# Optimization experiments

Measured on AMD Instinct MI355X. Metric: run time of the kernel, lower is better.

## Reference

```python
import jax, jax.numpy as jnp
import numpy as np

NUM_HEADS = 16
EPS = 1e-5
CHUNK = 128  # chunk length for the chunked recurrent-state scan


def _linear_attention(x, Wq, Wk, Wv, Wo, bo):
    B, T, E = x.shape
    H = NUM_HEADS
    d = E // H

    def proj(W):
        # nn.Linear(bias=False): y = x @ W.T ; split heads -> (B,H,T,d)
        return (x @ W.T).reshape(B, T, H, d).transpose(0, 2, 1, 3)

    phi_q = jax.nn.elu(proj(Wq)) + 1.0
    phi_k = jax.nn.elu(proj(Wk)) + 1.0
    V = proj(Wv)

    nC = T // CHUNK
    # (nC, B, H, C, d) so lax.scan iterates over chunks of time
    def to_chunks(a):
        return a.reshape(B, H, nC, CHUNK, d).transpose(2, 0, 1, 3, 4)

    qc, kc, vc = to_chunks(phi_q), to_chunks(phi_k), to_chunks(V)
    mask = jnp.tril(jnp.ones((CHUNK, CHUNK), x.dtype))  # causal incl. diagonal

    S0 = jnp.zeros((B, H, d, d), x.dtype)  # running sum of k v^T
    z0 = jnp.zeros((B, H, d), x.dtype)     # running sum of phi_k

    def step(carry, inp):
        S, z = carry
        q, k, v = inp  # (B,H,C,d)
        A = jnp.einsum('bhid,bhjd->bhij', q, k) * mask
        num = jnp.einsum('bhij,bhjd->bhid', A, v) + jnp.einsum('bhid,bhde->bhie', q, S)
        den = jnp.sum(A, axis=-1) + jnp.einsum('bhid,bhd->bhi', q, z) + EPS
        out = num / den[..., None]
        S = S + jnp.einsum('bhjd,bhje->bhde', k, v)
        z = z + jnp.sum(k, axis=2)
        return (S, z), out

    _, outs = jax.lax.scan(step, (S0, z0), (qc, kc, vc))  # (nC,B,H,C,d)
    out = outs.transpose(1, 2, 0, 3, 4).reshape(B, H, T, d)
    out = out.transpose(0, 2, 1, 3).reshape(B, T, E)
    # out_proj (dropout p=0 / eval -> identity)
    return out @ Wo.T + bo


def setup_inputs() -> dict:
    key = jax.random.key(0)
    ks = jax.random.split(key, 6)
    B, T, E = 2, 2048, 1024
    s = 1.0 / np.sqrt(E)
    return {
        'x': jax.random.normal(ks[0], (B, T, E), jnp.float32),
        'Wq': jax.random.normal(ks[1], (E, E), jnp.float32) * s,
        'Wk': jax.random.normal(ks[2], (E, E), jnp.float32) * s,
        'Wv': jax.random.normal(ks[3], (E, E), jnp.float32) * s,
        'Wo': jax.random.normal(ks[4], (E, E), jnp.float32) * s,
        'bo': jnp.zeros((E,), jnp.float32),
    }


def reference(x, Wq, Wk, Wv, Wo, bo):
    return _linear_attention(x, Wq, Wk, Wv, Wo, bo)
```

## Files before the change

kernel.cpp:

```cpp
#include <hip/hip_runtime.h>
#include <hip/hip_bf16.h>
#include <stdint.h>

typedef __attribute__((ext_vector_type(4)))  float  floatx4;
typedef __attribute__((ext_vector_type(8)))  short  short8;
typedef __attribute__((ext_vector_type(8)))  unsigned short ushortx8;
typedef __attribute__((ext_vector_type(4)))  unsigned short ushortx4;

#define B_  2
#define T_  2048
#define E_  1024
#define H_  16
#define D_  64
#define C_  128
#define NC_ 16
#define M_  4096
#define EPS_ 1e-5f

__device__ __forceinline__ unsigned short f2b(float f) {
    union { float f; unsigned int u; } v; v.f = f;
    unsigned int r = v.u + 0x7fffu + ((v.u >> 16) & 1u);
    return (unsigned short)(r >> 16);
}
__device__ __forceinline__ float b2f(unsigned short b) {
    union { unsigned int u; float f; } v; v.u = ((unsigned int)b) << 16;
    return v.f;
}

__device__ __forceinline__ int stage_seg(int i) { return (i & 3) ^ ((i >> 3) & 3); }
__device__ __forceinline__ int frag_slot(int lane) {
    int m = lane & 15, q = lane >> 4;
    return m * 4 + (q ^ ((m >> 1) & 3));
}

__global__ __launch_bounds__(256) void convert_all(const float* __restrict__ x,
                                                   const float* __restrict__ Wq,
                                                   const float* __restrict__ Wk,
                                                   const float* __restrict__ Wv,
                                                   const float* __restrict__ Wo,
                                                   unsigned short* __restrict__ dst) {
    int i = (blockIdx.x * 256 + threadIdx.x) * 4;
    const float* s; int off;
    if (i < M_ * E_) { s = x; off = i; }
    else {
        int j = i - M_ * E_;
        int which = j >> 20;
        s = (which == 0) ? Wq : (which == 1) ? Wk : (which == 2) ? Wv : Wo;
        off = j & ((1 << 20) - 1);
    }
    float4 f = *(const float4*)(s + off);
    ushortx4 o;
    o[0] = f2b(f.x); o[1] = f2b(f.y); o[2] = f2b(f.z); o[3] = f2b(f.w);
    *(ushortx4*)(dst + i) = o;
}

__global__ __launch_bounds__(256) void gemm_qkv(const unsigned short* __restrict__ A,
                                                const unsigned short* __restrict__ Bm,
                                                unsigned short* __restrict__ Cb) {
    const int N = 3 * E_, K = E_;
    __shared__ __align__(16) unsigned short smem[32768];
    unsigned short* at0 = smem;
    unsigned short* bt0 = smem + 8192;
    unsigned short* at1 = smem + 16384;
    unsigned short* bt1 = smem + 24576;
    int tid = threadIdx.x;
    int wave = tid >> 6, lane = tid & 63;
    int wr = wave >> 1, wc = wave & 1;
    int m = lane & 15, q = lane >> 4;
    int srow = lane >> 2, sseg = stage_seg(lane);
    int fs = frag_slot(lane);
    int row0 = blockIdx.y * 128, col0 = blockIdx.x * 128;
    floatx4 acc[4][4];
    for (int i = 0; i < 4; i++) for (int j = 0; j < 4; j++) acc[i][j] = floatx4{0.f, 0.f, 0.f, 0.f};

    auto stageA = [&](unsigned short* at, int k0) {
        for (int p = 0; p < 4; p++) {
            int t = p * 4 + wave;
            const unsigned short* ga = A + (size_t)(row0 + (t & 7) * 16 + srow) * K + k0 + (t >> 3) * 32 + sseg * 8;
            __builtin_amdgcn_global_load_lds((const __attribute__((address_space(1))) unsigned int*)ga,
                (__attribute__((address_space(3))) unsigned int*)(at + t * 512), 16, 0, 0);
        }
    };
    auto stageB = [&](unsigned short* bt, int k0) {
        for (int p = 0; p < 4; p++) {
            int u = p * 4 + wave;
            const unsigned short* gb = Bm + (size_t)(col0 + (u & 7) * 16 + srow) * K + k0 + (u >> 3) * 32 + sseg * 8;
            __builtin_amdgcn_global_load_lds((const __attribute__((address_space(1))) unsigned int*)gb,
                (__attribute__((address_space(3))) unsigned int*)(bt + u * 512), 16, 0, 0);
        }
    };
    short8 af[4], bf[4];
    auto frags = [&](const unsigned short* at, const unsigned short* bt, int kh) {
        for (int mi = 0; mi < 4; mi++) af[mi] = *(const short8*)(at + (kh * 8 + wr * 4 + mi) * 512 + fs * 8);
        for (int ni = 0; ni < 4; ni++) bf[ni] = *(const short8*)(bt + (kh * 8 + wc * 4 + ni) * 512 + fs * 8);
    };
    auto mfma16 = [&]() {
        __builtin_amdgcn_s_setprio(1);
        for (int mi = 0; mi < 4; mi++)
            for (int ni = 0; ni < 4; ni++)
                acc[mi][ni] = __builtin_amdgcn_mfma_f32_16x16x32_bf16(af[mi], bf[ni], acc[mi][ni], 0, 0, 0);
        __builtin_amdgcn_s_setprio(0);
    };

    stageA(at0, 0); stageB(bt0, 0);
    for (int k0 = 0; k0 < K; k0 += 128) {
        stageA(at1, k0 + 64);
        asm volatile("s_waitcnt vmcnt(4)" ::: "memory");
        __builtin_amdgcn_s_barrier();
        frags(at0, bt0, 0);
        mfma16();
        frags(at0, bt0, 1);
        stageB(bt1, k0 + 64);
        mfma16();
        __builtin_amdgcn_s_barrier();
        if (k0 + 128 < K) {
            stageA(at0, k0 + 128);
            asm volatile("s_waitcnt vmcnt(4)" ::: "memory");
        } else {
            asm volatile("s_waitcnt vmcnt(0)" ::: "memory");
        }
        __builtin_amdgcn_s_barrier();
        frags(at1, bt1, 0);
        mfma16();
        frags(at1, bt1, 1);
        if (k0 + 128 < K) stageB(bt0, k0 + 128);
        mfma16();
        __builtin_amdgcn_s_barrier();
    }

    unsigned short* epi = smem + wave * 2176;
    bool isphi = (col0 < 2 * E_);
    for (int half = 0; half < 2; half++) {
        if (half) asm volatile("" ::: "memory");
        for (int mi2 = 0; mi2 < 2; mi2++) {
            int mi = half * 2 + mi2;
            for (int ni = 0; ni < 4; ni++)
                for (int reg = 0; reg < 4; reg++) {
                    int lr = mi2 * 16 + q * 4 + reg;
                    float v = acc[mi][ni][reg];
                    if (isphi) v = (v > 0.f) ? (v + 1.f) : __expf(v);
                    epi[lr * 68 + ni * 16 + m] = f2b(v);
                }
        }
        for (int i = 0; i < 4; i++) {
            int s = i * 64 + lane;
            int lr = s >> 3, seg = s & 7;
            const unsigned short* p = epi + lr * 68 + seg * 8;
            ushortx4 lo = *(const ushortx4*)(p);
            ushortx4 hi = *(const ushortx4*)(p + 4);
            ushortx8 val;
            for (int e = 0; e < 4; e++) { val[e] = lo[e]; val[e + 4] = hi[e]; }
            int row = row0 + wr * 64 + half * 32 + lr;
            int col = col0 + wc * 64 + seg * 8;
            *(ushortx8*)(Cb + (size_t)row * N + col) = val;
        }
    }
}

__global__ __launch_bounds__(256) void gemm_out(const unsigned short* __restrict__ A,
                                                const unsigned short* __restrict__ Bm,
                                                const float* __restrict__ bias,
                                                float* __restrict__ Cf) {
    const int N = E_, K = E_;
    __shared__ __align__(16) unsigned short smem[24576];
    unsigned short* at0 = smem;
    unsigned short* bt0 = smem + 8192;
    unsigned short* at1 = smem + 12288;
    unsigned short* bt1 = smem + 20480;
    int tid = threadIdx.x;
    int wave = tid >> 6, lane = tid & 63;
    int wr = wave >> 1, wc = wave & 1;
    int m = lane & 15, q = lane >> 4;
    int srow = lane >> 2, sseg = stage_seg(lane);
    int fs = frag_slot(lane);
    int row0 = blockIdx.y * 128, col0 = blockIdx.x * 64;
    floatx4 acc[4][2];
    for (int i = 0; i < 4; i++) for (int j = 0; j < 2; j++) acc[i][j] = floatx4{0.f, 0.f, 0.f, 0.f};

    auto stageA = [&](unsigned short* at, int k0) {
        for (int p = 0; p < 4; p++) {
            int t = p * 4 + wave;
            const unsigned short* ga = A + (size_t)(row0 + (t & 7) * 16 + srow) * K + k0 + (t >> 3) * 32 + sseg * 8;
            __builtin_amdgcn_global_load_lds((const __attribute__((address_space(1))) unsigned int*)ga,
                (__attribute__((address_space(3))) unsigned int*)(at + t * 512), 16, 0, 0);
        }
    };
    auto stageB = [&](unsigned short* bt, int k0) {
        for (int p = 0; p < 2; p++) {
            int u = p * 4 + wave;
            const unsigned short* gb = Bm + (size_t)(col0 + (u & 3) * 16 + srow) * K + k0 + (u >> 2) * 32 + sseg * 8;
            __builtin_amdgcn_global_load_lds((const __attribute__((address_space(1))) unsigned int*)gb,
                (__attribute__((address_space(3))) unsigned int*)(bt + u * 512), 16, 0, 0);
        }
    };
    short8 af[4], bf[2];
    auto frags = [&](const unsigned short* at, const unsigned short* bt, int kh) {
        for (int mi = 0; mi < 4; mi++) af[mi] = *(const short8*)(at + (kh * 8 + wr * 4 + mi) * 512 + fs * 8);
        for (int ci = 0; ci < 2; ci++) bf[ci] = *(const short8*)(bt + (kh * 4 + wc * 2 + ci) * 512 + fs * 8);
    };
    auto mfma8 = [&]() {
        __builtin_amdgcn_s_setprio(1);
        for (int mi = 0; mi < 4; mi++)
            for (int ci = 0; ci < 2; ci++)
                acc[mi][ci] = __builtin_amdgcn_mfma_f32_16x16x32_bf16(af[mi], bf[ci], acc[mi][ci], 0, 0, 0);
        __builtin_amdgcn_s_setprio(0);
    };

    stageA(at0, 0); stageB(bt0, 0);
    for (int k0 = 0; k0 < K; k0 += 128) {
        stageA(at1, k0 + 64);
        asm volatile("s_waitcnt vmcnt(4)" ::: "memory");
        __builtin_amdgcn_s_barrier();
        frags(at0, bt0, 0);
        mfma8();
        frags(at0, bt0, 1);
        stageB(bt1, k0 + 64);
        mfma8();
        __builtin_amdgcn_s_barrier();
        if (k0 + 128 < K) {
            stageA(at0, k0 + 128);
            asm volatile("s_waitcnt vmcnt(4)" ::: "memory");
        } else {
            asm volatile("s_waitcnt vmcnt(0)" ::: "memory");
        }
        __builtin_amdgcn_s_barrier();
        frags(at1, bt1, 0);
        mfma8();
        frags(at1, bt1, 1);
        if (k0 + 128 < K) stageB(bt0, k0 + 128);
        mfma8();
        __builtin_amdgcn_s_barrier();
    }

    int qrow = q * 4;
    for (int ci = 0; ci < 2; ci++) {
        int col = col0 + wc * 32 + ci * 16 + m;
        float bv = bias[col];
        for (int mi = 0; mi < 4; mi++)
            for (int r2 = 0; r2 < 4; r2++) {
                int row = row0 + wr * 64 + mi * 16 + qrow + r2;
                Cf[(size_t)row * N + col] = acc[mi][ci][r2] + bv;
            }
    }
}

__global__ __launch_bounds__(256) void chunk_sums(const unsigned short* __restrict__ qkv,
                                                  float* __restrict__ Sc, float* __restrict__ zc) {
    int c = blockIdx.x, h = blockIdx.y, bb = blockIdx.z;
    __shared__ __align__(16) unsigned short Kt[64 * 132];
    __shared__ __align__(16) unsigned short Vt[80 * 132];
    int tid = threadIdx.x;
    int lane = tid & 63, w = tid >> 6;
    size_t rowb = (size_t)bb * T_ + (size_t)c * C_;
    int kcol = E_ + h * D_, vcol = 2 * E_ + h * D_;

    {
        int r4 = (tid >> 3) * 4;
        int seg = (tid & 7) * 8;
        ushortx8 kv[4], vv[4];
        for (int t = 0; t < 4; t++) {
            size_t g = (rowb + r4 + t) * 3072;
            kv[t] = *(const ushortx8*)(qkv + g + kcol + seg);
            vv[t] = *(const ushortx8*)(qkv + g + vcol + seg);
        }
        for (int e = 0; e < 8; e++) {
            ushortx4 ka, va;
            for (int t = 0; t < 4; t++) { ka[t] = kv[t][e]; va[t] = vv[t][e]; }
            *(ushortx4*)(Kt + (seg + e) * 132 + r4) = ka;
            *(ushortx4*)(Vt + (seg + e) * 132 + r4) = va;
        }
    }
    if (tid < 128) Vt[64 * 132 + tid] = 0x3f80;
    __syncthreads();

    floatx4 acc[5];
    for (int ni = 0; ni < 5; ni++) acc[ni] = floatx4{0.f, 0.f, 0.f, 0.f};
    int lm = lane & 15, lk = (lane >> 4) * 8;
    for (int k0 = 0; k0 < 128; k0 += 32) {
        short8 af = *(const short8*)(Kt + (w * 16 + lm) * 132 + k0 + lk);
        for (int ni = 0; ni < 5; ni++) {
            short8 bf = *(const short8*)(Vt + (ni * 16 + lm) * 132 + k0 + lk);
            acc[ni] = __builtin_amdgcn_mfma_f32_16x16x32_bf16(af, bf, acc[ni], 0, 0, 0);
        }
    }
    size_t base = ((size_t)(bb * H_ + h) * NC_ + c) * (size_t)(D_ * D_);
    int r0 = w * 16 + (lane >> 4) * 4;
    for (int ni = 0; ni < 4; ni++)
        for (int reg = 0; reg < 4; reg++)
            Sc[base + (size_t)(r0 + reg) * D_ + ni * 16 + lm] = acc[ni][reg];
    if (lm == 0) {
        size_t zb = ((size_t)(bb * H_ + h) * NC_ + c) * D_;
        for (int reg = 0; reg < 4; reg++) zc[zb + r0 + reg] = acc[4][reg];
    }
}

__global__ __launch_bounds__(256) void attn_kernel(const unsigned short* __restrict__ qkv,
                                                   const float* __restrict__ Sc,
                                                   const float* __restrict__ zc,
                                                   unsigned short* __restrict__ attn) {
    int c = blockIdx.x, h = blockIdx.y, bb = blockIdx.z;
    __shared__ __align__(16) unsigned short qs[128 * 68];
    __shared__ __align__(16) unsigned short ks[128 * 68];
    __shared__ __align__(16) unsigned short vt[64 * 132];
    __shared__ __align__(16) unsigned short ovl[128 * 36];
    __shared__ float zsh[64];
    int tid = threadIdx.x;
    int lane = tid & 63, w = tid >> 6;
    int lm = lane & 15, lq = lane >> 4;
    size_t rowb = (size_t)bb * T_ + (size_t)c * C_;
    int qcol = h * D_, kcol = E_ + h * D_, vcol = 2 * E_ + h * D_;

    for (int s = 0; s < 4; s++) {
        int off = s * 256 + tid;
        int r = off >> 3, seg = (off & 7) * 8;
        size_t g = (rowb + r) * 3072;
        ushortx8 q8 = *(const ushortx8*)(qkv + g + qcol + seg);
        ushortx8 k8 = *(const ushortx8*)(qkv + g + kcol + seg);
        *(ushortx8*)(qs + r * 68 + seg) = q8;
        *(ushortx8*)(ks + r * 68 + seg) = k8;
    }
    {
        int r4 = (tid >> 3) * 4;
        int seg = (tid & 7) * 8;
        ushortx8 vv[4];
        for (int t = 0; t < 4; t++)
            vv[t] = *(const ushortx8*)(qkv + (rowb + r4 + t) * 3072 + vcol + seg);
        for (int e = 0; e < 8; e++) {
            ushortx4 va;
            for (int t = 0; t < 4; t++) va[t] = vv[t][e];
            *(ushortx4*)(vt + (seg + e) * 132 + r4) = va;
        }
    }
    {
        size_t scb = ((size_t)(bb * H_ + h) * NC_) * (size_t)(D_ * D_);
        int p = tid * 16;
        float a[16];
        for (int i = 0; i < 16; i++) a[i] = 0.f;
        for (int j = 0; j < c; j++) {
            const float* Sj = Sc + scb + (size_t)j * (D_ * D_) + p;
            for (int q = 0; q < 16; q += 4) {
                float4 f = *(const float4*)(Sj + q);
                a[q] += f.x; a[q + 1] += f.y; a[q + 2] += f.z; a[q + 3] += f.w;
            }
        }
        for (int i = 0; i < 16; i++) {
            int d = (p + i) >> 6, e = (p + i) & 63;
            ovl[e * 68 + d] = f2b(a[i]);
        }
    }
    if (tid < 64) {
        size_t zb = ((size_t)(bb * H_ + h) * NC_) * D_;
        float zr = 0.f;
        for (int j = 0; j < c; j++) zr += zc[zb + (size_t)j * D_ + tid];
        zsh[tid] = zr;
    }
    __syncthreads();

    floatx4 acc[2][4];
    for (int mi = 0; mi < 2; mi++) for (int ni = 0; ni < 4; ni++) acc[mi][ni] = floatx4{0.f, 0.f, 0.f, 0.f};
    for (int k0 = 0; k0 < 64; k0 += 32) {
        short8 aq[2];
        for (int mi = 0; mi < 2; mi++)
            aq[mi] = *(const short8*)(qs + (w * 32 + mi * 16 + lm) * 68 + k0 + lq * 8);
        for (int ni = 0; ni < 4; ni++) {
            short8 bs = *(const short8*)(ovl + (ni * 16 + lm) * 68 + k0 + lq * 8);
            for (int mi = 0; mi < 2; mi++)
                acc[mi][ni] = __builtin_amdgcn_mfma_f32_16x16x32_bf16(aq[mi], bs, acc[mi][ni], 0, 0, 0);
        }
    }
    float dsum[2][4];
    {
        int d0 = lm * 4;
        float4 z4 = *(const float4*)(zsh + d0);
        for (int mi = 0; mi < 2; mi++)
            for (int reg = 0; reg < 4; reg++) {
                int row = w * 32 + mi * 16 + lq * 4 + reg;
                ushortx4 q4 = *(const ushortx4*)(qs + row * 68 + d0);
                dsum[mi][reg] = b2f(q4[0]) * z4.x + b2f(q4[1]) * z4.y + b2f(q4[2]) * z4.z + b2f(q4[3]) * z4.w;
            }
    }
    __syncthreads();

    for (int jt = 0; jt <= w; jt++) {
        floatx4 pa[2][2];
        for (int mi = 0; mi < 2; mi++) for (int ct = 0; ct < 2; ct++) pa[mi][ct] = floatx4{0.f, 0.f, 0.f, 0.f};
        for (int k0 = 0; k0 < 64; k0 += 32) {
            short8 aq[2];
            for (int mi = 0; mi < 2; mi++)
                aq[mi] = *(const short8*)(qs + (w * 32 + mi * 16 + lm) * 68 + k0 + lq * 8);
            for (int ct = 0; ct < 2; ct++) {
                short8 bk = *(const short8*)(ks + (jt * 32 + ct * 16 + lm) * 68 + k0 + lq * 8);
                for (int mi = 0; mi < 2; mi++)
                    pa[mi][ct] = __builtin_amdgcn_mfma_f32_16x16x32_bf16(aq[mi], bk, pa[mi][ct], 0, 0, 0);
            }
        }
        bool diag = (jt == w);
        for (int mi = 0; mi < 2; mi++)
            for (int ct = 0; ct < 2; ct++)
                for (int reg = 0; reg < 4; reg++) {
                    int il = mi * 16 + lq * 4 + reg;
                    int jl = ct * 16 + lm;
                    float v = pa[mi][ct][reg];
                    if (diag && jl > il) v = 0.f;
                    dsum[mi][reg] += v;
                    ovl[(w * 32 + il) * 36 + jl] = f2b(v);
                }
        short8 ap[2];
        for (int mi = 0; mi < 2; mi++)
            ap[mi] = *(const short8*)(ovl + (w * 32 + mi * 16 + lm) * 36 + lq * 8);
        for (int ni = 0; ni < 4; ni++) {
            short8 bv = *(const short8*)(vt + (ni * 16 + lm) * 132 + jt * 32 + lq * 8);
            for (int mi = 0; mi < 2; mi++)
                acc[mi][ni] = __builtin_amdgcn_mfma_f32_16x16x32_bf16(ap[mi], bv, acc[mi][ni], 0, 0, 0);
        }
    }

    for (int off = 1; off < 16; off <<= 1)
        for (int mi = 0; mi < 2; mi++)
            for (int reg = 0; reg < 4; reg++)
                dsum[mi][reg] += __shfl_xor(dsum[mi][reg], off);

    for (int mi = 0; mi < 2; mi++)
        for (int reg = 0; reg < 4; reg++) {
            float inv = 1.f / (dsum[mi][reg] + EPS_);
            int row = w * 32 + mi * 16 + lq * 4 + reg;
            for (int ni = 0; ni < 4; ni++)
                attn[(rowb + row) * E_ + h * D_ + ni * 16 + lm] = f2b(acc[mi][ni][reg] * inv);
        }
}

extern "C" void kernel_launch(void* const* d_in, const int* in_sizes, int n_in,
                              void* d_out, int out_size, void* d_ws, size_t ws_size,
                              hipStream_t stream) {
    const float* x  = (const float*)d_in[0];
    const float* Wq = (const float*)d_in[1];
    const float* Wk = (const float*)d_in[2];
    const float* Wv = (const float*)d_in[3];
    const float* Wo = (const float*)d_in[4];
    const float* bo = (const float*)d_in[5];
    float* out = (float*)d_out;

    const size_t MB = 1024 * 1024;
    uint8_t* ws = (uint8_t*)d_ws;
    unsigned short* xb    = (unsigned short*)(ws + 0);
    unsigned short* wb    = (unsigned short*)(ws + 8 * MB);
    unsigned short* wob   = wb + 3 * E_ * E_;
    unsigned short* qkvb  = (unsigned short*)(ws + 16 * MB);
    float* Sc = (float*)(ws + 40 * MB);
    float* zc = (float*)(ws + 48 * MB);
    unsigned short* attnb = xb;

    convert_all<<<(M_ * E_ + 4 * E_ * E_) / 1024, 256, 0, stream>>>(x, Wq, Wk, Wv, Wo, xb);

    gemm_qkv<<<dim3(24, 32), 256, 0, stream>>>(xb, wb, qkvb);
    chunk_sums<<<dim3(NC_, H_, B_), 256, 0, stream>>>(qkvb, Sc, zc);
    attn_kernel<<<dim3(NC_, H_, B_), 256, 0, stream>>>(qkvb, Sc, zc, attnb);
    gemm_out<<<dim3(16, 32), 256, 0, stream>>>(attnb, wob, bo, out);
}
```

Baseline: 161.5 us.

## Precompute exclusive prefix state per chunk in separate kernel; load Q fragments directly

Adds a prefix_state kernel that computes, once per (batch, head), the exclusive prefix sums of the per-chunk KV states and key sums. It stores the KV prefixes as transposed bf16 and the key-sum prefixes as fp32. Before this, each attention block re-summed all earlier chunk states on its own. The attention kernel now reads its precomputed prefix directly and loads Q fragments from global memory into registers, dropping the Q LDS tile. The trade-off is an extra serial, low-parallelism launch (32 blocks) with strided transposed stores. It also reuses the weight workspace region for the prefix buffers.

```diff
diff --git a/kernel.cpp b/kernel.cpp
--- a/kernel.cpp
+++ b/kernel.cpp
@@ -294,29 +294,55 @@
     }
 }
 
+__global__ __launch_bounds__(256) void prefix_state(const float* __restrict__ Sc,
+                                                    const float* __restrict__ zc,
+                                                    unsigned short* __restrict__ Spt,
+                                                    float* __restrict__ zp) {
+    int h = blockIdx.x, bb = blockIdx.y;
+    int tid = threadIdx.x;
+    size_t bh = (size_t)bb * H_ + h;
+    const float* S = Sc + bh * NC_ * (size_t)(D_ * D_);
+    unsigned short* P = Spt + bh * NC_ * (size_t)(D_ * D_);
+    int p = tid * 16, r = p >> 6, c0 = p & 63;
+    float a[16];
+    for (int i = 0; i < 16; i++) a[i] = 0.f;
+    for (int cc = 0; cc < NC_; cc++) {
+        unsigned short* Pc = P + (size_t)cc * (D_ * D_);
+        for (int i = 0; i < 16; i++)
+            Pc[(c0 + i) * D_ + r] = f2b(a[i]);
+        const float* Sj = S + (size_t)cc * (D_ * D_) + p;
+        for (int q = 0; q < 16; q += 4) {
+            float4 f = *(const float4*)(Sj + q);
+            a[q] += f.x; a[q + 1] += f.y; a[q + 2] += f.z; a[q + 3] += f.w;
+        }
+    }
+    if (tid < 64) {
+        const float* z = zc + bh * NC_ * (size_t)D_;
+        float* zo = zp + bh * NC_ * (size_t)D_;
+        float za = 0.f;
+        for (int cc = 0; cc < NC_; cc++) { zo[cc * D_ + tid] = za; za += z[cc * D_ + tid]; }
+    }
+}
+
 __global__ __launch_bounds__(256) void attn_kernel(const unsigned short* __restrict__ qkv,
-                                                   const float* __restrict__ Sc,
-                                                   const float* __restrict__ zc,
+                                                   const unsigned short* __restrict__ Spt,
+                                                   const float* __restrict__ zp,
                                                    unsigned short* __restrict__ attn) {
     int c = blockIdx.x, h = blockIdx.y, bb = blockIdx.z;
-    __shared__ __align__(16) unsigned short qs[128 * 68];
     __shared__ __align__(16) unsigned short ks[128 * 68];
     __shared__ __align__(16) unsigned short vt[64 * 132];
     __shared__ __align__(16) unsigned short ovl[128 * 36];
-    __shared__ float zsh[64];
     int tid = threadIdx.x;
     int lane = tid & 63, w = tid >> 6;
     int lm = lane & 15, lq = lane >> 4;
     size_t rowb = (size_t)bb * T_ + (size_t)c * C_;
     int qcol = h * D_, kcol = E_ + h * D_, vcol = 2 * E_ + h * D_;
+    size_t pbase = ((size_t)bb * H_ + h) * NC_ + c;
 
     for (int s = 0; s < 4; s++) {
         int off = s * 256 + tid;
         int r = off >> 3, seg = (off & 7) * 8;
-        size_t g = (rowb + r) * 3072;
-        ushortx8 q8 = *(const ushortx8*)(qkv + g + qcol + seg);
-        ushortx8 k8 = *(const ushortx8*)(qkv + g + kcol + seg);
-        *(ushortx8*)(qs + r * 68 + seg) = q8;
+        ushortx8 k8 = *(const ushortx8*)(qkv + (rowb + r) * 3072 + kcol + seg);
         *(ushortx8*)(ks + r * 68 + seg) = k8;
     }
     {
@@ -331,51 +357,30 @@
             *(ushortx4*)(vt + (seg + e) * 132 + r4) = va;
         }
     }
-    {
-        size_t scb = ((size_t)(bb * H_ + h) * NC_) * (size_t)(D_ * D_);
-        int p = tid * 16;
-        float a[16];
-        for (int i = 0; i < 16; i++) a[i] = 0.f;
-        for (int j = 0; j < c; j++) {
-            const float* Sj = Sc + scb + (size_t)j * (D_ * D_) + p;
-            for (int q = 0; q < 16; q += 4) {
-                float4 f = *(const float4*)(Sj + q);
-                a[q] += f.x; a[q + 1] += f.y; a[q + 2] += f.z; a[q + 3] += f.w;
-            }
-        }
-        for (int i = 0; i < 16; i++) {
-            int d = (p + i) >> 6, e = (p + i) & 63;
-            ovl[e * 68 + d] = f2b(a[i]);
-        }
-    }
-    if (tid < 64) {
-        size_t zb = ((size_t)(bb * H_ + h) * NC_) * D_;
-        float zr = 0.f;
-        for (int j = 0; j < c; j++) zr += zc[zb + (size_t)j * D_ + tid];
-        zsh[tid] = zr;
-    }
-    __syncthreads();
+
+    short8 aq[2][2];
+    for (int mi = 0; mi < 2; mi++)
+        for (int kk = 0; kk < 2; kk++)
+            aq[mi][kk] = *(const short8*)(qkv + (rowb + w * 32 + mi * 16 + lm) * 3072 + qcol + kk * 32 + lq * 8);
 
     floatx4 acc[2][4];
     for (int mi = 0; mi < 2; mi++) for (int ni = 0; ni < 4; ni++) acc[mi][ni] = floatx4{0.f, 0.f, 0.f, 0.f};
-    for (int k0 = 0; k0 < 64; k0 += 32) {
-        short8 aq[2];
-        for (int mi = 0; mi < 2; mi++)
-            aq[mi] = *(const short8*)(qs + (w * 32 + mi * 16 + lm) * 68 + k0 + lq * 8);
-        for (int ni = 0; ni < 4; ni++) {
-            short8 bs = *(const short8*)(ovl + (ni * 16 + lm) * 68 + k0 + lq * 8);
-            for (int mi = 0; mi < 2; mi++)
-                acc[mi][ni] = __builtin_amdgcn_mfma_f32_16x16x32_bf16(aq[mi], bs, acc[mi][ni], 0, 0, 0);
-        }
+    {
+        const unsigned short* sp = Spt + pbase * (size_t)(D_ * D_);
+        for (int kk = 0; kk < 2; kk++)
+            for (int ni = 0; ni < 4; ni++) {
+                short8 bs = *(const short8*)(sp + (ni * 16 + lm) * D_ + kk * 32 + lq * 8);
+                for (int mi = 0; mi < 2; mi++)
+                    acc[mi][ni] = __builtin_amdgcn_mfma_f32_16x16x32_bf16(aq[mi][kk], bs, acc[mi][ni], 0, 0, 0);
+            }
     }
     float dsum[2][4];
     {
-        int d0 = lm * 4;
-        float4 z4 = *(const float4*)(zsh + d0);
+        float4 z4 = *(const float4*)(zp + pbase * D_ + lm * 4);
         for (int mi = 0; mi < 2; mi++)
             for (int reg = 0; reg < 4; reg++) {
                 int row = w * 32 + mi * 16 + lq * 4 + reg;
-                ushortx4 q4 = *(const ushortx4*)(qs + row * 68 + d0);
+                ushortx4 q4 = *(const ushortx4*)(qkv + (rowb + row) * 3072 + qcol + lm * 4);
                 dsum[mi][reg] = b2f(q4[0]) * z4.x + b2f(q4[1]) * z4.y + b2f(q4[2]) * z4.z + b2f(q4[3]) * z4.w;
             }
     }
@@ -384,16 +389,12 @@
     for (int jt = 0; jt <= w; jt++) {
         floatx4 pa[2][2];
         for (int mi = 0; mi < 2; mi++) for (int ct = 0; ct < 2; ct++) pa[mi][ct] = floatx4{0.f, 0.f, 0.f, 0.f};
-        for (int k0 = 0; k0 < 64; k0 += 32) {
-            short8 aq[2];
-            for (int mi = 0; mi < 2; mi++)
-                aq[mi] = *(const short8*)(qs + (w * 32 + mi * 16 + lm) * 68 + k0 + lq * 8);
+        for (int kk = 0; kk < 2; kk++)
             for (int ct = 0; ct < 2; ct++) {
-                short8 bk = *(const short8*)(ks + (jt * 32 + ct * 16 + lm) * 68 + k0 + lq * 8);
+                short8 bk = *(const short8*)(ks + (jt * 32 + ct * 16 + lm) * 68 + kk * 32 + lq * 8);
                 for (int mi = 0; mi < 2; mi++)
-                    pa[mi][ct] = __builtin_amdgcn_mfma_f32_16x16x32_bf16(aq[mi], bk, pa[mi][ct], 0, 0, 0);
+                    pa[mi][ct] = __builtin_amdgcn_mfma_f32_16x16x32_bf16(aq[mi][kk], bk, pa[mi][ct], 0, 0, 0);
             }
-        }
         bool diag = (jt == w);
         for (int mi = 0; mi < 2; mi++)
             for (int ct = 0; ct < 2; ct++)
@@ -449,11 +450,14 @@
     float* Sc = (float*)(ws + 40 * MB);
     float* zc = (float*)(ws + 48 * MB);
     unsigned short* attnb = xb;
+    unsigned short* sptb  = wb;
+    float* zpb            = (float*)(ws + 12 * MB);
 
     convert_all<<<(M_ * E_ + 4 * E_ * E_) / 1024, 256, 0, stream>>>(x, Wq, Wk, Wv, Wo, xb);
 
     gemm_qkv<<<dim3(24, 32), 256, 0, stream>>>(xb, wb, qkvb);
     chunk_sums<<<dim3(NC_, H_, B_), 256, 0, stream>>>(qkvb, Sc, zc);
-    attn_kernel<<<dim3(NC_, H_, B_), 256, 0, stream>>>(qkvb, Sc, zc, attnb);
+    prefix_state<<<dim3(H_, B_), 256, 0, stream>>>(Sc, zc, sptb, zpb);
+    attn_kernel<<<dim3(NC_, H_, B_), 256, 0, stream>>>(qkvb, sptb, zpb, attnb);
     gemm_out<<<dim3(16, 32), 256, 0, stream>>>(attnb, wob, bo, out);
 }
```

Result: no change. 164.2 us (+1.7%).
